# Kernel optimization log

Measured on AMD Instinct MI355X. Metric: run time of the kernel, lower is better.

The kernel has to match this reference:

```python
import jax, jax.numpy as jnp
import numpy as np

B, L, D = 8, 2048, 512
H, P = 8, 4
C = D // H  # dim_per_head


def setup_inputs() -> dict:
    key = jax.random.key(0)
    ks = jax.random.split(key, 11)
    sc = lambda k, shape, s=0.02: jax.random.normal(k, shape, jnp.float32) * s
    return dict(
        query=jax.random.normal(ks[0], (B, L, D), jnp.float32),
        key_in=jax.random.normal(ks[1], (B, L, D), jnp.float32),
        value=jax.random.normal(ks[2], (B, L, D), jnp.float32),
        W_v=sc(ks[3], (D, D)), b_v=jnp.zeros((D,), jnp.float32),
        W_off=sc(ks[4], (D, H * P * 2), 0.01), b_off=sc(ks[5], (H * P * 2,), 0.2),
        W_aw=sc(ks[6], (D, H * P), 0.01), b_aw=jnp.zeros((H * P,), jnp.float32),
        W_out=sc(ks[7], (D, D)), b_out=jnp.zeros((D,), jnp.float32),
    )


def reference(query, key_in, value, W_v, b_v, W_off, b_off, W_aw, b_aw, W_out, b_out):
    # value projection
    v = value @ W_v + b_v                                        # (B,L,D)
    # sampling offsets and attention weights from the query
    off = (query @ W_off + b_off).reshape(B, L, H, P, 2)         # (B,L,H,P,2)
    aw = jax.nn.softmax((query @ W_aw + b_aw).reshape(B, L, H, P), axis=-1)
    # reference point for query i is (x=linspace[0]=0, y=linspace[i]) because
    # the torch code slices reference_points[:, :, :, :1, :]
    ref_y = jnp.linspace(0.0, 1.0, L, dtype=jnp.float32)
    loc_x = jnp.clip(off[..., 0], 0.0, 1.0)                      # ref_x = 0
    loc_y = jnp.clip(off[..., 1] + ref_y[None, :, None, None], 0.0, 1.0)
    # grid_sample, align_corners=False, input (BH, C, 1, L)
    ix = ((loc_x + 1.0) * L - 1.0) * 0.5                         # width coord in [ (L-1)/2, L-0.5 ]
    iy = loc_y * 0.5                                             # ((y+1)*1 - 1)/2
    ix0 = jnp.floor(ix)
    fx = ix - ix0
    iy0 = jnp.floor(iy)
    fy = iy - iy0
    # height dim has size 1: row iy0 valid iff ==0, row iy0+1 valid iff ==0 (zero padding)
    ywt = (1.0 - fy) * (iy0 == 0.0).astype(jnp.float32) + fy * ((iy0 + 1.0) == 0.0).astype(jnp.float32)
    i0 = ix0.astype(jnp.int32)
    i1 = i0 + 1

    perm = lambda a: a.transpose(0, 2, 1, 3)                     # (B,L,H,P) -> (B,H,L,P)
    i0p, i1p = perm(i0), perm(i1)
    vh = v.reshape(B, L, H, C).transpose(0, 2, 1, 3)             # (B,H,L,C)

    gather = jax.vmap(jax.vmap(lambda vm, ii: vm[ii]))           # (L,C),(L,P) -> (L,P,C)
    m0 = ((i0p >= 0) & (i0p < L)).astype(jnp.float32)[..., None]
    m1 = ((i1p >= 0) & (i1p < L)).astype(jnp.float32)[..., None]
    g0 = gather(vh, jnp.clip(i0p, 0, L - 1)) * m0                # (B,H,L,P,C)
    g1 = gather(vh, jnp.clip(i1p, 0, L - 1)) * m1

    fxp = perm(fx)[..., None]
    ywtp = perm(ywt)[..., None]
    samp = ywtp * ((1.0 - fxp) * g0 + fxp * g1)                  # (B,H,L,P,C)
    out = (samp * perm(aw)[..., None]).sum(axis=3)               # (B,H,L,C)
    out = out.transpose(0, 2, 1, 3).reshape(B, L, D)
    return out @ W_out + b_out
```

## Files before the change

### kernel.cpp

```cpp
#include <hip/hip_runtime.h>
#include <stdint.h>

#define M_ROWS 16384
#define PSZF (16384 * 96)

using short8  = __attribute__((ext_vector_type(8))) short;
using floatx4 = __attribute__((ext_vector_type(4))) float;

__device__ __forceinline__ unsigned short f2bf(float f) {
  union { float f; unsigned u; } v; v.f = f;
  unsigned r = v.u + 0x7fffu + ((v.u >> 16) & 1u);
  return (unsigned short)(r >> 16);
}
__device__ __forceinline__ float bf2f(unsigned short u) {
  union { unsigned u; float f; } v; v.u = ((unsigned)u) << 16; return v.f;
}

__device__ __forceinline__ void load_lds16(const unsigned short* g, unsigned short* l) {
  __builtin_amdgcn_global_load_lds(
      (const __attribute__((address_space(1))) unsigned int*)g,
      (__attribute__((address_space(3))) unsigned int*)l, 16, 0, 0);
}

__device__ __forceinline__ void store_val(float* p, float v) { *p = v; }
__device__ __forceinline__ void store_val(unsigned short* p, float v) { *p = f2bf(v); }


__global__ __launch_bounds__(256) void conv_bf16(const float* __restrict__ src,
                                                 unsigned short* __restrict__ dst, int n4) {
  int i = blockIdx.x * 256 + threadIdx.x;
  if (i >= n4) return;
  float4 v = ((const float4*)src)[i];
  ushort4 o;
  o.x = f2bf(v.x); o.y = f2bf(v.y); o.z = f2bf(v.z); o.w = f2bf(v.w);
  ((ushort4*)dst)[i] = o;
}

__global__ __launch_bounds__(256) void transpose_bf16(const float* __restrict__ src,
                                                      unsigned short* __restrict__ dst) {
  int idx = blockIdx.x * 256 + threadIdx.x;
  int n = idx >> 9, k = idx & 511;
  dst[idx] = f2bf(src[(k << 9) + n]);
}

__global__ __launch_bounds__(256) void buildcat(const float* __restrict__ Woff,
                                                const float* __restrict__ Waw,
                                                const float* __restrict__ boff,
                                                const float* __restrict__ baw,
                                                unsigned short* __restrict__ Bhi,
                                                unsigned short* __restrict__ Blo,
                                                float* __restrict__ bcat) {
  int idx = blockIdx.x * 256 + threadIdx.x;
  if (idx < 96 * 512) {
    int n = idx >> 9, k = idx & 511;
    float w = (n < 64) ? Woff[(k << 6) + n] : Waw[(k << 5) + (n - 64)];
    unsigned short hi = f2bf(w);
    Bhi[idx] = hi;
    Blo[idx] = f2bf(w - bf2f(hi));
  }
  if (idx < 96) bcat[idx] = (idx < 64) ? boff[idx] : baw[idx - 64];
}

template <typename OutT>
__global__ __launch_bounds__(256) void gemm_bt(const unsigned short* __restrict__ A,
                                               const unsigned short* __restrict__ Bt,
                                               const float* __restrict__ bias,
                                               OutT* __restrict__ C, int N, int K) {
  __shared__ __align__(16) unsigned short lA[128 * 32];
  __shared__ __align__(16) unsigned short lB[128 * 32];
  int tid  = threadIdx.x;
  int lane = tid & 63, wv = tid >> 6;
  int wm = wv & 1, wn = wv >> 1;
  int lrow = lane & 15, quad = lane >> 4;
  int rowBlk = blockIdx.y * 128, colBlk = blockIdx.x * 128;

  const unsigned short* Ab = A + (size_t)rowBlk * K;
  const unsigned short* Bb = Bt + (size_t)colBlk * K;
  int r0 = tid >> 2;
  int c0 = (tid & 3) << 3;

  floatx4 acc[4][4];
#pragma unroll
  for (int i = 0; i < 4; i++)
#pragma unroll
    for (int j = 0; j < 4; j++) acc[i][j] = (floatx4){0.f, 0.f, 0.f, 0.f};

  for (int k0 = 0; k0 < K; k0 += 32) {
    load_lds16(Ab + (size_t)r0 * K + k0 + c0,        lA + tid * 8);
    load_lds16(Ab + (size_t)(r0 + 64) * K + k0 + c0, lA + 2048 + tid * 8);
    load_lds16(Bb + (size_t)r0 * K + k0 + c0,        lB + tid * 8);
    load_lds16(Bb + (size_t)(r0 + 64) * K + k0 + c0, lB + 2048 + tid * 8);
    __syncthreads();

    short8 a[4], b[4];
#pragma unroll
    for (int mi = 0; mi < 4; mi++)
      a[mi] = *(const short8*)&lA[(wm * 64 + mi * 16 + lrow) * 32 + quad * 8];
#pragma unroll
    for (int ni = 0; ni < 4; ni++)
      b[ni] = *(const short8*)&lB[(wn * 64 + ni * 16 + lrow) * 32 + quad * 8];
#pragma unroll
    for (int mi = 0; mi < 4; mi++)
#pragma unroll
      for (int ni = 0; ni < 4; ni++)
        acc[mi][ni] = __builtin_amdgcn_mfma_f32_16x16x32_bf16(a[mi], b[ni], acc[mi][ni], 0, 0, 0);
    __syncthreads();
  }

#pragma unroll
  for (int ni = 0; ni < 4; ni++) {
    int col = colBlk + wn * 64 + ni * 16 + lrow;
    float bv = bias[col];
#pragma unroll
    for (int mi = 0; mi < 4; mi++) {
      int row = rowBlk + wm * 64 + mi * 16 + quad * 4;
#pragma unroll
      for (int r = 0; r < 4; r++)
        store_val(&C[(size_t)(row + r) * N + col], acc[mi][ni][r] + bv);
    }
  }
}

__global__ __launch_bounds__(128) void offaw_mfma(const float* __restrict__ Q,
                                                  const unsigned short* __restrict__ Bhi,
                                                  const unsigned short* __restrict__ Blo,
                                                  const float* __restrict__ bcat,
                                                  float* __restrict__ P) {
  __shared__ __align__(16) unsigned short lA[64 * 32];
  __shared__ __align__(16) unsigned short lB[96 * 32];
  int seg = blockIdx.x;
  int row0 = blockIdx.y * 64;
  int tid = threadIdx.x;
  int lane = tid & 63, wn = tid >> 6;
  int lrow = lane & 15, quad = lane >> 4;
  const unsigned short* Bt = (seg == 1) ? Blo : Bhi;
  bool wantlo = (seg == 2);
  float* out = P + (size_t)seg * PSZF;

  int ar = tid >> 1;
  int ach = (tid & 1) << 4;

  floatx4 acc[4][3];
#pragma unroll
  for (int i = 0; i < 4; i++)
#pragma unroll
    for (int j = 0; j < 3; j++) acc[i][j] = (floatx4){0.f, 0.f, 0.f, 0.f};

  const float* qrow = Q + (size_t)(row0 + ar) * 512 + ach;

  for (int k0 = 0; k0 < 512; k0 += 32) {
#pragma unroll
    for (int j = 0; j < 4; j++) {
      float4 v = *(const float4*)(qrow + k0 + j * 4);
      if (wantlo) {
        v.x -= bf2f(f2bf(v.x)); v.y -= bf2f(f2bf(v.y));
        v.z -= bf2f(f2bf(v.z)); v.w -= bf2f(f2bf(v.w));
      }
      ushort4 o;
      o.x = f2bf(v.x); o.y = f2bf(v.y); o.z = f2bf(v.z); o.w = f2bf(v.w);
      *(ushort4*)&lA[ar * 32 + ach + j * 4] = o;
    }
#pragma unroll
    for (int j = 0; j < 3; j++) {
      int e = tid + j * 128;
      int n = e >> 2, c = (e & 3) << 3;
      load_lds16(Bt + (size_t)n * 512 + k0 + c, lB + e * 8);
    }
    __syncthreads();

    short8 a[4], b[3];
#pragma unroll
    for (int mi = 0; mi < 4; mi++)
      a[mi] = *(const short8*)&lA[(mi * 16 + lrow) * 32 + quad * 8];
#pragma unroll
    for (int ni = 0; ni < 3; ni++)
      b[ni] = *(const short8*)&lB[(wn * 48 + ni * 16 + lrow) * 32 + quad * 8];
#pragma unroll
    for (int mi = 0; mi < 4; mi++)
#pragma unroll
      for (int ni = 0; ni < 3; ni++)
        acc[mi][ni] = __builtin_amdgcn_mfma_f32_16x16x32_bf16(a[mi], b[ni], acc[mi][ni], 0, 0, 0);
    __syncthreads();
  }

#pragma unroll
  for (int ni = 0; ni < 3; ni++) {
    int col = wn * 48 + ni * 16 + lrow;
    float bv = (seg == 0) ? bcat[col] : 0.0f;
#pragma unroll
    for (int mi = 0; mi < 4; mi++) {
      int row = row0 + mi * 16 + quad * 4;
#pragma unroll
      for (int r = 0; r < 4; r++)
        out[(size_t)(row + r) * 96 + col] = acc[mi][ni][r] + bv;
    }
  }
}

__global__ __launch_bounds__(256) void sample_kernel(const float* __restrict__ P,
                                                     const unsigned short* __restrict__ v,
                                                     unsigned short* __restrict__ attn) {
  int row = blockIdx.x;
  int b = row >> 11, l = row & 2047;
  __shared__ float s_w0[32], s_w1[32];
  __shared__ int s_i0[32], s_i1[32];
  int tid = threadIdx.x;

  if (tid < 32) {
    int base = row * 96;
    float lg = P[base + 64 + tid] + P[PSZF + base + 64 + tid] + P[2 * PSZF + base + 64 + tid];
    float mx = fmaxf(lg, __shfl_xor(lg, 1));
    mx = fmaxf(mx, __shfl_xor(mx, 2));
    float e = __expf(lg - mx);
    float s = e + __shfl_xor(e, 1);
    s = s + __shfl_xor(s, 2);
    float aw = e / s;

    float ox = P[base + 2 * tid] + P[PSZF + base + 2 * tid] + P[2 * PSZF + base + 2 * tid];
    float oy = P[base + 2 * tid + 1] + P[PSZF + base + 2 * tid + 1] + P[2 * PSZF + base + 2 * tid + 1];
    float refy = (float)l * (1.0f / 2047.0f);
    float lx = fminf(fmaxf(ox, 0.0f), 1.0f);
    float ly = fminf(fmaxf(oy + refy, 0.0f), 1.0f);
    float ix = ((lx + 1.0f) * 2048.0f - 1.0f) * 0.5f;
    float ywt = 1.0f - ly * 0.5f;
    float ix0 = floorf(ix);
    float fx = ix - ix0;
    int i0 = (int)ix0;
    int i1 = i0 + 1;
    s_w0[tid] = aw * ywt * (1.0f - fx);
    s_w1[tid] = (i1 < 2048) ? (aw * ywt * fx) : 0.0f;
    s_i0[tid] = i0;
    s_i1[tid] = (i1 < 2048) ? i1 : 2047;
  }
  __syncthreads();

  const unsigned short* vb = v + ((size_t)(b << 11)) * 512;
  int c = tid & 63;
#pragma unroll
  for (int hh = 0; hh < 2; hh++) {
    int h = (tid >> 6) + (hh << 2);
    const unsigned short* vhc = vb + h * 64 + c;
    float acc = 0.0f;
#pragma unroll
    for (int p = 0; p < 4; p++) {
      int t = (h << 2) + p;
      acc += s_w0[t] * bf2f(vhc[(size_t)s_i0[t] << 9]) +
             s_w1[t] * bf2f(vhc[(size_t)s_i1[t] << 9]);
    }
    attn[(size_t)row * 512 + h * 64 + c] = f2bf(acc);
  }
}

extern "C" void kernel_launch(void* const* d_in, const int* in_sizes, int n_in,
                              void* d_out, int out_size, void* d_ws, size_t ws_size,
                              hipStream_t stream) {
  (void)in_sizes; (void)n_in; (void)out_size; (void)ws_size;
  const float* query = (const float*)d_in[0];
  const float* value = (const float*)d_in[2];
  const float* W_v   = (const float*)d_in[3];
  const float* b_v   = (const float*)d_in[4];
  const float* W_off = (const float*)d_in[5];
  const float* b_off = (const float*)d_in[6];
  const float* W_aw  = (const float*)d_in[7];
  const float* b_aw  = (const float*)d_in[8];
  const float* W_out = (const float*)d_in[9];
  const float* b_out = (const float*)d_in[10];
  float* out = (float*)d_out;

  char* ws = (char*)d_ws;
  const size_t MB = 1ull << 20;
  unsigned short* val_bf = (unsigned short*)(ws);
  unsigned short* attn   = val_bf;
  unsigned short* v_bf   = (unsigned short*)(ws + 16 * MB);
  float* offP            = (float*)(ws + 32 * MB);
  unsigned short* Wv_t   = (unsigned short*)(ws + 50 * MB);
  unsigned short* Wo_t   = (unsigned short*)(ws + 50 * MB + 524288);
  unsigned short* Bhi    = (unsigned short*)(ws + 51 * MB);
  unsigned short* Blo    = (unsigned short*)(ws + 51 * MB + 98304);
  float* bcat            = (float*)(ws + 51 * MB + 196608);

  conv_bf16<<<8192, 256, 0, stream>>>(value, val_bf, 2097152);
  transpose_bf16<<<1024, 256, 0, stream>>>(W_v, Wv_t);
  transpose_bf16<<<1024, 256, 0, stream>>>(W_out, Wo_t);
  buildcat<<<192, 256, 0, stream>>>(W_off, W_aw, b_off, b_aw, Bhi, Blo, bcat);

  gemm_bt<unsigned short><<<dim3(4, 128), 256, 0, stream>>>(val_bf, Wv_t, b_v, v_bf, 512, 512);
  offaw_mfma<<<dim3(3, 256), 128, 0, stream>>>(query, Bhi, Blo, bcat, offP);
  sample_kernel<<<16384, 256, 0, stream>>>(offP, v_bf, attn);
  gemm_bt<float><<<dim3(4, 128), 256, 0, stream>>>(attn, Wo_t, b_out, out, 512, 512);
}
```

Before: 231.1 us.

## Fuse prep kernels, precompute split-bf16 query, split-K offset GEMM, vectorize sampling

Merges the value conversion and a new query hi/lo split into one kernel, and the three weight-prep kernels into one, cutting launch count. The offset/attention-weight GEMM now reads the pre-split bf16 query through direct-to-LDS loads. It runs all three hi/lo MFMA products inside one block with a split-K over two halves, producing two partial planes instead of three. The sampling kernel gathers two bf16 channels per thread with 32-bit loads. The cost is an extra round trip of the query through global memory in bf16 hi/lo form.

Measured after the change: 217.9 us. 1.06x faster.

```diff
diff --git a/kernel.cpp b/kernel.cpp
--- a/kernel.cpp
+++ b/kernel.cpp
@@ -25,40 +25,59 @@
 __device__ __forceinline__ void store_val(float* p, float v) { *p = v; }
 __device__ __forceinline__ void store_val(unsigned short* p, float v) { *p = f2bf(v); }
 
-
-__global__ __launch_bounds__(256) void conv_bf16(const float* __restrict__ src,
-                                                 unsigned short* __restrict__ dst, int n4) {
+__global__ __launch_bounds__(256) void conv_all(const float* __restrict__ value,
+                                                const float* __restrict__ query,
+                                                unsigned short* __restrict__ val_bf,
+                                                unsigned short* __restrict__ Qhi,
+                                                unsigned short* __restrict__ Qlo) {
   int i = blockIdx.x * 256 + threadIdx.x;
-  if (i >= n4) return;
-  float4 v = ((const float4*)src)[i];
-  ushort4 o;
-  o.x = f2bf(v.x); o.y = f2bf(v.y); o.z = f2bf(v.z); o.w = f2bf(v.w);
-  ((ushort4*)dst)[i] = o;
-}
-
-__global__ __launch_bounds__(256) void transpose_bf16(const float* __restrict__ src,
-                                                      unsigned short* __restrict__ dst) {
+  if (i < 2097152) {
+    float4 v = ((const float4*)value)[i];
+    ushort4 o;
+    o.x = f2bf(v.x); o.y = f2bf(v.y); o.z = f2bf(v.z); o.w = f2bf(v.w);
+    ((ushort4*)val_bf)[i] = o;
+  } else {
+    int j = i - 2097152;
+    float4 v = ((const float4*)query)[j];
+    ushort4 hi, lo;
+    hi.x = f2bf(v.x); hi.y = f2bf(v.y); hi.z = f2bf(v.z); hi.w = f2bf(v.w);
+    lo.x = f2bf(v.x - bf2f(hi.x)); lo.y = f2bf(v.y - bf2f(hi.y));
+    lo.z = f2bf(v.z - bf2f(hi.z)); lo.w = f2bf(v.w - bf2f(hi.w));
+    ((ushort4*)Qhi)[j] = hi;
+    ((ushort4*)Qlo)[j] = lo;
+  }
+}
+
+__global__ __launch_bounds__(256) void prep_w(const float* __restrict__ W_v,
+                                              const float* __restrict__ W_out,
+                                              const float* __restrict__ Woff,
+                                              const float* __restrict__ Waw,
+                                              const float* __restrict__ boff,
+                                              const float* __restrict__ baw,
+                                              unsigned short* __restrict__ Wv_t,
+                                              unsigned short* __restrict__ Wo_t,
+                                              unsigned short* __restrict__ Bhi,
+                                              unsigned short* __restrict__ Blo,
+                                              float* __restrict__ bcat) {
   int idx = blockIdx.x * 256 + threadIdx.x;
-  int n = idx >> 9, k = idx & 511;
-  dst[idx] = f2bf(src[(k << 9) + n]);
-}
-
-__global__ __launch_bounds__(256) void buildcat(const float* __restrict__ Woff,
-                                                const float* __restrict__ Waw,
-                                                const float* __restrict__ boff,
-                                                const float* __restrict__ baw,
-                                                unsigned short* __restrict__ Bhi,
-                                                unsigned short* __restrict__ Blo,
-                                                float* __restrict__ bcat) {
-  int idx = blockIdx.x * 256 + threadIdx.x;
-  if (idx < 96 * 512) {
+  if (idx < 262144) {
     int n = idx >> 9, k = idx & 511;
+    Wv_t[idx] = f2bf(W_v[(k << 9) + n]);
+  } else if (idx < 524288) {
+    int t = idx - 262144;
+    int n = t >> 9, k = t & 511;
+    Wo_t[t] = f2bf(W_out[(k << 9) + n]);
+  } else if (idx < 524288 + 49152) {
+    int t = idx - 524288;
+    int n = t >> 9, k = t & 511;
     float w = (n < 64) ? Woff[(k << 6) + n] : Waw[(k << 5) + (n - 64)];
     unsigned short hi = f2bf(w);
-    Bhi[idx] = hi;
-    Blo[idx] = f2bf(w - bf2f(hi));
-  }
-  if (idx < 96) bcat[idx] = (idx < 64) ? boff[idx] : baw[idx - 64];
+    Bhi[t] = hi;
+    Blo[t] = f2bf(w - bf2f(hi));
+  } else if (idx < 524288 + 49152 + 96) {
+    int t = idx - 524288 - 49152;
+    bcat[t] = (t < 64) ? boff[t] : baw[t - 64];
+  }
 }
 
 template <typename OutT>
@@ -121,75 +140,80 @@
   }
 }
 
-__global__ __launch_bounds__(128) void offaw_mfma(const float* __restrict__ Q,
-                                                  const unsigned short* __restrict__ Bhi,
-                                                  const unsigned short* __restrict__ Blo,
-                                                  const float* __restrict__ bcat,
-                                                  float* __restrict__ P) {
-  __shared__ __align__(16) unsigned short lA[64 * 32];
-  __shared__ __align__(16) unsigned short lB[96 * 32];
-  int seg = blockIdx.x;
+__global__ __launch_bounds__(256) void offaw2(const unsigned short* __restrict__ Qhi,
+                                              const unsigned short* __restrict__ Qlo,
+                                              const unsigned short* __restrict__ Bhi,
+                                              const unsigned short* __restrict__ Blo,
+                                              const float* __restrict__ bcat,
+                                              float* __restrict__ P) {
+  __shared__ __align__(16) unsigned short lAhi[64 * 32];
+  __shared__ __align__(16) unsigned short lAlo[64 * 32];
+  __shared__ __align__(16) unsigned short lBhi[96 * 32];
+  __shared__ __align__(16) unsigned short lBlo[96 * 32];
+  int khalf = blockIdx.x;
   int row0 = blockIdx.y * 64;
   int tid = threadIdx.x;
-  int lane = tid & 63, wn = tid >> 6;
+  int lane = tid & 63, wv = tid >> 6;
+  int wm = wv & 1, wn = wv >> 1;
   int lrow = lane & 15, quad = lane >> 4;
-  const unsigned short* Bt = (seg == 1) ? Blo : Bhi;
-  bool wantlo = (seg == 2);
-  float* out = P + (size_t)seg * PSZF;
-
-  int ar = tid >> 1;
-  int ach = (tid & 1) << 4;
-
-  floatx4 acc[4][3];
-#pragma unroll
-  for (int i = 0; i < 4; i++)
+  int kbase = khalf << 8;
+
+  int an = tid >> 2, ac = (tid & 3) << 3;
+  const unsigned short* qhb = Qhi + (size_t)(row0 + an) * 512 + kbase + ac;
+  const unsigned short* qlb = Qlo + (size_t)(row0 + an) * 512 + kbase + ac;
+  int bn = tid >> 2, bc = (tid & 3) << 3;
+  int e2 = 256 + tid;
+  int bn2 = e2 >> 2, bc2 = (e2 & 3) << 3;
+
+  floatx4 acc[2][3];
+#pragma unroll
+  for (int i = 0; i < 2; i++)
 #pragma unroll
     for (int j = 0; j < 3; j++) acc[i][j] = (floatx4){0.f, 0.f, 0.f, 0.f};
 
-  const float* qrow = Q + (size_t)(row0 + ar) * 512 + ach;
-
-  for (int k0 = 0; k0 < 512; k0 += 32) {
-#pragma unroll
-    for (int j = 0; j < 4; j++) {
-      float4 v = *(const float4*)(qrow + k0 + j * 4);
-      if (wantlo) {
-        v.x -= bf2f(f2bf(v.x)); v.y -= bf2f(f2bf(v.y));
-        v.z -= bf2f(f2bf(v.z)); v.w -= bf2f(f2bf(v.w));
+  for (int k0 = 0; k0 < 256; k0 += 32) {
+    load_lds16(qhb + k0, lAhi + tid * 8);
+    load_lds16(qlb + k0, lAlo + tid * 8);
+    load_lds16(Bhi + (size_t)bn * 512 + kbase + k0 + bc, lBhi + tid * 8);
+    load_lds16(Blo + (size_t)bn * 512 + kbase + k0 + bc, lBlo + tid * 8);
+    if (tid < 128) {
+      load_lds16(Bhi + (size_t)bn2 * 512 + kbase + k0 + bc2, lBhi + e2 * 8);
+      load_lds16(Blo + (size_t)bn2 * 512 + kbase + k0 + bc2, lBlo + e2 * 8);
+    }
+    __syncthreads();
+
+    short8 ah[2], al[2], bh[3], bl[3];
+#pragma unroll
+    for (int mi = 0; mi < 2; mi++) {
+      int r = (wm * 32 + mi * 16 + lrow) * 32 + quad * 8;
+      ah[mi] = *(const short8*)&lAhi[r];
+      al[mi] = *(const short8*)&lAlo[r];
+    }
+#pragma unroll
+    for (int ni = 0; ni < 3; ni++) {
+      int r = (wn * 48 + ni * 16 + lrow) * 32 + quad * 8;
+      bh[ni] = *(const short8*)&lBhi[r];
+      bl[ni] = *(const short8*)&lBlo[r];
+    }
+#pragma unroll
+    for (int mi = 0; mi < 2; mi++)
+#pragma unroll
+      for (int ni = 0; ni < 3; ni++) {
+        acc[mi][ni] = __builtin_amdgcn_mfma_f32_16x16x32_bf16(ah[mi], bh[ni], acc[mi][ni], 0, 0, 0);
+        acc[mi][ni] = __builtin_amdgcn_mfma_f32_16x16x32_bf16(ah[mi], bl[ni], acc[mi][ni], 0, 0, 0);
+        acc[mi][ni] = __builtin_amdgcn_mfma_f32_16x16x32_bf16(al[mi], bh[ni], acc[mi][ni], 0, 0, 0);
       }
-      ushort4 o;
-      o.x = f2bf(v.x); o.y = f2bf(v.y); o.z = f2bf(v.z); o.w = f2bf(v.w);
-      *(ushort4*)&lA[ar * 32 + ach + j * 4] = o;
-    }
-#pragma unroll
-    for (int j = 0; j < 3; j++) {
-      int e = tid + j * 128;
-      int n = e >> 2, c = (e & 3) << 3;
-      load_lds16(Bt + (size_t)n * 512 + k0 + c, lB + e * 8);
-    }
     __syncthreads();
-
-    short8 a[4], b[3];
-#pragma unroll
-    for (int mi = 0; mi < 4; mi++)
-      a[mi] = *(const short8*)&lA[(mi * 16 + lrow) * 32 + quad * 8];
-#pragma unroll
-    for (int ni = 0; ni < 3; ni++)
-      b[ni] = *(const short8*)&lB[(wn * 48 + ni * 16 + lrow) * 32 + quad * 8];
-#pragma unroll
-    for (int mi = 0; mi < 4; mi++)
-#pragma unroll
-      for (int ni = 0; ni < 3; ni++)
-        acc[mi][ni] = __builtin_amdgcn_mfma_f32_16x16x32_bf16(a[mi], b[ni], acc[mi][ni], 0, 0, 0);
-    __syncthreads();
-  }
-
+  }
+
+  float* out = P + (size_t)khalf * PSZF;
 #pragma unroll
   for (int ni = 0; ni < 3; ni++) {
     int col = wn * 48 + ni * 16 + lrow;
-    float bv = (seg == 0) ? bcat[col] : 0.0f;
-#pragma unroll
-    for (int mi = 0; mi < 4; mi++) {
-      int row = row0 + mi * 16 + quad * 4;
+    float bv = (khalf == 0) ? bcat[col] : 0.0f;
+#pragma unroll
+    for (int mi = 0; mi < 2; mi++) {
+      int row = row0 + wm * 32 + mi * 16 + quad * 4;
 #pragma unroll
       for (int r = 0; r < 4; r++)
         out[(size_t)(row + r) * 96 + col] = acc[mi][ni][r] + bv;
@@ -208,7 +232,7 @@
 
   if (tid < 32) {
     int base = row * 96;
-    float lg = P[base + 64 + tid] + P[PSZF + base + 64 + tid] + P[2 * PSZF + base + 64 + tid];
+    float lg = P[base + 64 + tid] + P[PSZF + base + 64 + tid];
     float mx = fmaxf(lg, __shfl_xor(lg, 1));
     mx = fmaxf(mx, __shfl_xor(mx, 2));
     float e = __expf(lg - mx);
@@ -216,8 +240,8 @@
     s = s + __shfl_xor(s, 2);
     float aw = e / s;
 
-    float ox = P[base + 2 * tid] + P[PSZF + base + 2 * tid] + P[2 * PSZF + base + 2 * tid];
-    float oy = P[base + 2 * tid + 1] + P[PSZF + base + 2 * tid + 1] + P[2 * PSZF + base + 2 * tid + 1];
+    float ox = P[base + 2 * tid] + P[PSZF + base + 2 * tid];
+    float oy = P[base + 2 * tid + 1] + P[PSZF + base + 2 * tid + 1];
     float refy = (float)l * (1.0f / 2047.0f);
     float lx = fminf(fmaxf(ox, 0.0f), 1.0f);
     float ly = fminf(fmaxf(oy + refy, 0.0f), 1.0f);
@@ -235,20 +259,20 @@
   __syncthreads();
 
   const unsigned short* vb = v + ((size_t)(b << 11)) * 512;
-  int c = tid & 63;
-#pragma unroll
-  for (int hh = 0; hh < 2; hh++) {
-    int h = (tid >> 6) + (hh << 2);
-    const unsigned short* vhc = vb + h * 64 + c;
-    float acc = 0.0f;
-#pragma unroll
-    for (int p = 0; p < 4; p++) {
-      int t = (h << 2) + p;
-      acc += s_w0[t] * bf2f(vhc[(size_t)s_i0[t] << 9]) +
-             s_w1[t] * bf2f(vhc[(size_t)s_i1[t] << 9]);
-    }
-    attn[(size_t)row * 512 + h * 64 + c] = f2bf(acc);
-  }
+  int h = tid >> 5, c = (tid & 31) << 1;
+  const unsigned short* vhc = vb + h * 64 + c;
+  float ax = 0.0f, ay = 0.0f;
+#pragma unroll
+  for (int p = 0; p < 4; p++) {
+    int t = (h << 2) + p;
+    unsigned g0 = *(const unsigned*)(vhc + ((size_t)s_i0[t] << 9));
+    unsigned g1 = *(const unsigned*)(vhc + ((size_t)s_i1[t] << 9));
+    float w0 = s_w0[t], w1 = s_w1[t];
+    ax += w0 * bf2f((unsigned short)g0) + w1 * bf2f((unsigned short)g1);
+    ay += w0 * bf2f((unsigned short)(g0 >> 16)) + w1 * bf2f((unsigned short)(g1 >> 16));
+  }
+  unsigned packed = (unsigned)f2bf(ax) | ((unsigned)f2bf(ay) << 16);
+  *(unsigned*)(attn + (size_t)row * 512 + h * 64 + c) = packed;
 }
 
 extern "C" void kernel_launch(void* const* d_in, const int* in_sizes, int n_in,
@@ -272,20 +296,21 @@
   unsigned short* val_bf = (unsigned short*)(ws);
   unsigned short* attn   = val_bf;
   unsigned short* v_bf   = (unsigned short*)(ws + 16 * MB);
-  float* offP            = (float*)(ws + 32 * MB);
-  unsigned short* Wv_t   = (unsigned short*)(ws + 50 * MB);
-  unsigned short* Wo_t   = (unsigned short*)(ws + 50 * MB + 524288);
-  unsigned short* Bhi    = (unsigned short*)(ws + 51 * MB);
-  unsigned short* Blo    = (unsigned short*)(ws + 51 * MB + 98304);
-  float* bcat            = (float*)(ws + 51 * MB + 196608);
-
-  conv_bf16<<<8192, 256, 0, stream>>>(value, val_bf, 2097152);
-  transpose_bf16<<<1024, 256, 0, stream>>>(W_v, Wv_t);
-  transpose_bf16<<<1024, 256, 0, stream>>>(W_out, Wo_t);
-  buildcat<<<192, 256, 0, stream>>>(W_off, W_aw, b_off, b_aw, Bhi, Blo, bcat);
+  unsigned short* Qhi    = (unsigned short*)(ws + 32 * MB);
+  unsigned short* Qlo    = (unsigned short*)(ws + 48 * MB);
+  float* offP            = (float*)(ws + 64 * MB);
+  unsigned short* Wv_t   = (unsigned short*)(ws + 80 * MB);
+  unsigned short* Wo_t   = (unsigned short*)(ws + 80 * MB + 524288);
+  unsigned short* Bhi    = (unsigned short*)(ws + 81 * MB);
+  unsigned short* Blo    = (unsigned short*)(ws + 81 * MB + 98304);
+  float* bcat            = (float*)(ws + 81 * MB + 196608);
+
+  conv_all<<<16384, 256, 0, stream>>>(value, query, val_bf, Qhi, Qlo);
+  prep_w<<<2241, 256, 0, stream>>>(W_v, W_out, W_off, W_aw, b_off, b_aw,
+                                   Wv_t, Wo_t, Bhi, Blo, bcat);
 
   gemm_bt<unsigned short><<<dim3(4, 128), 256, 0, stream>>>(val_bf, Wv_t, b_v, v_bf, 512, 512);
-  offaw_mfma<<<dim3(3, 256), 128, 0, stream>>>(query, Bhi, Blo, bcat, offP);
+  offaw2<<<dim3(2, 256), 256, 0, stream>>>(Qhi, Qlo, Bhi, Blo, bcat, offP);
   sample_kernel<<<16384, 256, 0, stream>>>(offP, v_bf, attn);
   gemm_bt<float><<<dim3(4, 128), 256, 0, stream>>>(attn, Wo_t, b_out, out, 512, 512);
 }
```
